# Performance work log

Hardware: AMD Instinct MI355X
Metric: run time of the kernel (lower is better)

The kernel has to match this reference:

```python
import jax, jax.numpy as jnp
import numpy as np

DIM = 768
HEADS = 12
DH = DIM // HEADS
HIDDEN = 4 * DIM
EPS = 1e-5


def layernorm(x, g, b):
    mu = jnp.mean(x, axis=-1, keepdims=True)
    var = jnp.mean(jnp.square(x - mu), axis=-1, keepdims=True)
    return (x - mu) * jax.lax.rsqrt(var + EPS) * g + b


def setup_inputs() -> dict:
    key = jax.random.key(0)
    ks = jax.random.split(key, 12)
    B, N = 8, 1024
    s_in = 1.0 / np.sqrt(DIM)
    s_hid = 1.0 / np.sqrt(HIDDEN)
    return {
        "x": jax.random.normal(ks[0], (B, N, DIM), jnp.float32),
        "q_extra": jax.random.normal(ks[1], (B, N, DIM), jnp.float32),
        "ln1_g": jnp.ones((DIM,), jnp.float32),
        "ln1_b": jnp.zeros((DIM,), jnp.float32),
        "w_kv": jax.random.normal(ks[2], (DIM, 2 * DIM), jnp.float32) * s_in,
        "w_out": jax.random.normal(ks[3], (DIM, DIM), jnp.float32) * s_in,
        "b_out": jnp.zeros((DIM,), jnp.float32),
        "ln2_g": jnp.ones((DIM,), jnp.float32),
        "ln2_b": jnp.zeros((DIM,), jnp.float32),
        "w1": jax.random.normal(ks[4], (DIM, HIDDEN), jnp.float32) * s_in,
        "b1": jnp.zeros((HIDDEN,), jnp.float32),
        "w2": jax.random.normal(ks[5], (HIDDEN, DIM), jnp.float32) * s_hid,
        "b2": jnp.zeros((DIM,), jnp.float32),
    }


def reference(x, q_extra, ln1_g, ln1_b, w_kv, w_out, b_out, ln2_g, ln2_b, w1, b1, w2, b2):
    B, N, C = x.shape
    scale = DH ** (-0.5)

    # pre-norm cross attention
    xn = layernorm(x, ln1_g, ln1_b)
    kv = (xn @ w_kv).reshape(B, N, 2, HEADS, DH)
    k = kv[:, :, 0]  # [B,N,H,Dh]
    v = kv[:, :, 1]
    q = q_extra.reshape(B, N, HEADS, DH)
    dots = jnp.einsum('bnhd,bmhd->bhnm', q, k) * scale
    attn = jax.nn.softmax(dots, axis=-1)
    out = jnp.einsum('bhnm,bmhd->bnhd', attn, v).reshape(B, N, C)
    out = out @ w_out + b_out

    x = x + out  # residual

    # pre-norm MLP
    h = layernorm(x, ln2_g, ln2_b)
    h = jax.nn.gelu(h @ w1 + b1, approximate=False)
    h = h @ w2 + b2
    return x + h
```

## Files before the change

kernel.cpp:

```cpp
#include <hip/hip_runtime.h>
#include <math.h>

typedef __attribute__((ext_vector_type(8))) short short8;
typedef __attribute__((ext_vector_type(8))) _Float16 half8;
typedef __attribute__((ext_vector_type(2))) __fp16 fp16x2;
typedef __attribute__((ext_vector_type(4))) float float4v;
typedef __attribute__((ext_vector_type(4))) unsigned short ushort4v;

__device__ __forceinline__ unsigned short f2bf(float f) {
  union { unsigned int i; float f; } x; x.f = f;
  unsigned int r = x.i + 0x7fffu + ((x.i >> 16) & 1u);
  return (unsigned short)(r >> 16);
}

__device__ __forceinline__ float gelu_f(float y) {
  const float z = fabsf(y) * 0.70710678118654752f;
  const float t = 1.0f / (1.0f + 0.3275911f * z);
  const float poly = t * (0.254829592f + t * (-0.284496736f +
                     t * (1.421413741f + t * (-1.453152027f + t * 1.061405429f))));
  const float e = exp2f(-z * z * 1.44269504088896f);
  const float erfz = copysignf(1.0f - poly * e, y);
  return 0.5f * y * (1.0f + erfz);
}

__global__ void ln_kernel(const float* __restrict__ in, const float* __restrict__ g,
                          const float* __restrict__ b, unsigned short* __restrict__ out) {
  const int wave = threadIdx.x >> 6, lane = threadIdx.x & 63;
  const int row = blockIdx.x * 4 + wave;
  const float* xr = in + (size_t)row * 768 + lane * 4;
  const float4 v0 = *(const float4*)(xr);
  const float4 v1 = *(const float4*)(xr + 256);
  const float4 v2 = *(const float4*)(xr + 512);
  float s  = (v0.x + v0.y) + (v0.z + v0.w) + (v1.x + v1.y) + (v1.z + v1.w)
           + (v2.x + v2.y) + (v2.z + v2.w);
  float s2 = v0.x*v0.x + v0.y*v0.y + v0.z*v0.z + v0.w*v0.w
           + v1.x*v1.x + v1.y*v1.y + v1.z*v1.z + v1.w*v1.w
           + v2.x*v2.x + v2.y*v2.y + v2.z*v2.z + v2.w*v2.w;
  for (int off = 32; off > 0; off >>= 1) {
    s  += __shfl_xor(s, off, 64);
    s2 += __shfl_xor(s2, off, 64);
  }
  const float mu = s * (1.0f / 768.0f);
  const float var = s2 * (1.0f / 768.0f) - mu * mu;
  const float rstd = rsqrtf(var + 1e-5f);
  const float* gp = g + lane * 4;
  const float* bp = b + lane * 4;
  unsigned short* orow = out + (size_t)row * 768 + lane * 4;
#pragma unroll
  for (int k = 0; k < 3; ++k) {
    const float4 v = (k == 0) ? v0 : (k == 1) ? v1 : v2;
    const float4 gv = *(const float4*)(gp + k * 256);
    const float4 bv = *(const float4*)(bp + k * 256);
    ushort4v o;
    o.x = f2bf((v.x - mu) * rstd * gv.x + bv.x);
    o.y = f2bf((v.y - mu) * rstd * gv.y + bv.y);
    o.z = f2bf((v.z - mu) * rstd * gv.z + bv.z);
    o.w = f2bf((v.w - mu) * rstd * gv.w + bv.w);
    *(ushort4v*)(orow + k * 256) = o;
  }
}

__global__ void wtrans_kernel(const float* __restrict__ in, unsigned short* __restrict__ out,
                              int K, int N) {
  __shared__ float tile[32][33];
  const int k0 = blockIdx.y * 32, n0 = blockIdx.x * 32;
  const int tr = threadIdx.x >> 5, tc = threadIdx.x & 31;
#pragma unroll
  for (int i = 0; i < 4; ++i)
    tile[tr + i * 8][tc] = in[(size_t)(k0 + tr + i * 8) * N + n0 + tc];
  __syncthreads();
#pragma unroll
  for (int i = 0; i < 4; ++i)
    out[(size_t)(n0 + tr + i * 8) * K + k0 + tc] = f2bf(tile[tc][tr + i * 8]);
}

#define SWIZ_BLOCK(GX, TW)                                        \
  const int _id = (int)blockIdx.x;                                \
  const int _gy8 = (int)gridDim.x / (8 * (GX));                   \
  const int _xcd = _id & 7, _jj = _id >> 3;                       \
  const int row0 = (_xcd * _gy8 + _jj / (GX)) * 128;              \
  const int col0 = (_jj % (GX)) * (TW);

#define ASM_FENCE asm volatile("" ::: "memory")

__device__ __forceinline__ void gemm128(
    const unsigned short* __restrict__ A, int lda,
    const unsigned short* __restrict__ Bt, int ldb, int K,
    int row0, int col0,
    unsigned short* As, unsigned short* Bs,
    float4v acc[4][4]) {
  const int t = threadIdx.x, lane = t & 63, wave = t >> 6;
  const int quad = lane >> 4, l16 = lane & 15;
  const int wr = wave >> 1, wc = wave & 1;
  const int srow = lane >> 3;
  const int scol = ((lane & 7) ^ srow) * 8;
#pragma unroll
  for (int mt = 0; mt < 4; ++mt)
#pragma unroll
    for (int nt = 0; nt < 4; ++nt) acc[mt][nt] = (float4v)(0.0f);

  for (int kk = 0; kk < K; kk += 64) {
    __syncthreads();
#pragma unroll
    for (int j = 0; j < 4; ++j) {
      const int chunk = wave * 4 + j;
      const int r = chunk * 8 + srow;
      __builtin_amdgcn_global_load_lds(
          (const __attribute__((address_space(1))) unsigned int*)(A + (size_t)(row0 + r) * lda + kk + scol),
          (__attribute__((address_space(3))) unsigned int*)(As + chunk * 512),
          16, 0, 0);
      __builtin_amdgcn_global_load_lds(
          (const __attribute__((address_space(1))) unsigned int*)(Bt + (size_t)(col0 + r) * ldb + kk + scol),
          (__attribute__((address_space(3))) unsigned int*)(Bs + chunk * 512),
          16, 0, 0);
    }
    __syncthreads();
#pragma unroll
    for (int ks = 0; ks < 2; ++ks) {
      const int gsw = ((ks * 4 + quad) ^ (l16 & 7)) * 8;
      short8 af[4], bfv[4];
#pragma unroll
      for (int i = 0; i < 4; ++i) {
        af[i]  = *(const short8*)(As + (wr * 64 + i * 16 + l16) * 64 + gsw);
        bfv[i] = *(const short8*)(Bs + (wc * 64 + i * 16 + l16) * 64 + gsw);
      }
#pragma unroll
      for (int mt = 0; mt < 4; ++mt)
#pragma unroll
        for (int nt = 0; nt < 4; ++nt)
          acc[mt][nt] = __builtin_amdgcn_mfma_f32_16x16x32_bf16(af[mt], bfv[nt], acc[mt][nt], 0, 0, 0);
    }
  }
}

#define GEMM128_PROLOGUE(GX)                                     \
  __shared__ unsigned short As[128 * 64];                        \
  __shared__ unsigned short Bs[128 * 64];                        \
  float4v acc[4][4];                                             \
  SWIZ_BLOCK(GX, 128)                                            \
  const int t = threadIdx.x, lane = t & 63, wave = t >> 6;       \
  const int quad = lane >> 4, l16 = lane & 15;                   \
  const int wr = wave >> 1, wc = wave & 1; (void)t;

__device__ __forceinline__ void stage12864(
    const unsigned short* __restrict__ A, int lda,
    const unsigned short* __restrict__ Bt, int ldb,
    int row0, int col0, int kk,
    unsigned short* Asb, unsigned short* Bsb,
    int wave, int srow, int scol) {
#pragma unroll
  for (int j = 0; j < 4; ++j) {
    const int chunk = wave * 4 + j;
    const int r = chunk * 8 + srow;
    __builtin_amdgcn_global_load_lds(
        (const __attribute__((address_space(1))) unsigned int*)(A + (size_t)(row0 + r) * lda + kk + scol),
        (__attribute__((address_space(3))) unsigned int*)(Asb + chunk * 512),
        16, 0, 0);
  }
#pragma unroll
  for (int j = 0; j < 2; ++j) {
    const int chunk = wave * 2 + j;
    const int r = chunk * 8 + srow;
    __builtin_amdgcn_global_load_lds(
        (const __attribute__((address_space(1))) unsigned int*)(Bt + (size_t)(col0 + r) * ldb + kk + scol),
        (__attribute__((address_space(3))) unsigned int*)(Bsb + chunk * 512),
        16, 0, 0);
  }
}

__device__ __forceinline__ void mfma_step12864(
    const unsigned short* Ab, const unsigned short* Bb,
    int wave, int quad, int l16, float4v acc[2][4]) {
#pragma unroll
  for (int ks = 0; ks < 2; ++ks) {
    const int gsw = ((ks * 4 + quad) ^ (l16 & 7)) * 8;
    short8 af[2], bfv[4];
#pragma unroll
    for (int i = 0; i < 2; ++i)
      af[i] = *(const short8*)(Ab + (wave * 32 + i * 16 + l16) * 64 + gsw);
#pragma unroll
    for (int i = 0; i < 4; ++i)
      bfv[i] = *(const short8*)(Bb + (i * 16 + l16) * 64 + gsw);
#pragma unroll
    for (int mt = 0; mt < 2; ++mt)
#pragma unroll
      for (int nt = 0; nt < 4; ++nt)
        acc[mt][nt] = __builtin_amdgcn_mfma_f32_16x16x32_bf16(af[mt], bfv[nt], acc[mt][nt], 0, 0, 0);
  }
}

__device__ __forceinline__ void gemm12864(
    const unsigned short* __restrict__ A, int lda,
    const unsigned short* __restrict__ Bt, int ldb, int K,
    int row0, int col0,
    unsigned short* As, unsigned short* Bs,
    float4v acc[2][4]) {
  const int t = threadIdx.x, lane = t & 63, wave = t >> 6;
  const int quad = lane >> 4, l16 = lane & 15;
  const int srow = lane >> 3;
  const int scol = ((lane & 7) ^ srow) * 8;
#pragma unroll
  for (int mt = 0; mt < 2; ++mt)
#pragma unroll
    for (int nt = 0; nt < 4; ++nt) acc[mt][nt] = (float4v)(0.0f);

  stage12864(A, lda, Bt, ldb, row0, col0, 0, As, Bs, wave, srow, scol);
  stage12864(A, lda, Bt, ldb, row0, col0, 64, As + 8192, Bs + 4096, wave, srow, scol);

  for (int kk = 0; kk < K - 128; kk += 128) {
    asm volatile("s_waitcnt vmcnt(6)" ::: "memory");
    __builtin_amdgcn_s_barrier();
    ASM_FENCE;
    mfma_step12864(As, Bs, wave, quad, l16, acc);
    ASM_FENCE;
    __builtin_amdgcn_s_barrier();
    ASM_FENCE;
    stage12864(A, lda, Bt, ldb, row0, col0, kk + 128, As, Bs, wave, srow, scol);

    asm volatile("s_waitcnt vmcnt(6)" ::: "memory");
    __builtin_amdgcn_s_barrier();
    ASM_FENCE;
    mfma_step12864(As + 8192, Bs + 4096, wave, quad, l16, acc);
    ASM_FENCE;
    __builtin_amdgcn_s_barrier();
    ASM_FENCE;
    stage12864(A, lda, Bt, ldb, row0, col0, kk + 192, As + 8192, Bs + 4096, wave, srow, scol);
  }
  asm volatile("s_waitcnt vmcnt(6)" ::: "memory");
  __builtin_amdgcn_s_barrier();
  ASM_FENCE;
  mfma_step12864(As, Bs, wave, quad, l16, acc);
  asm volatile("s_waitcnt vmcnt(0)" ::: "memory");
  __builtin_amdgcn_s_barrier();
  ASM_FENCE;
  mfma_step12864(As + 8192, Bs + 4096, wave, quad, l16, acc);
}

#define GEMM12864_PROLOGUE(GX)                                   \
  __shared__ unsigned short As[2 * 128 * 64];                    \
  __shared__ unsigned short Bs[2 * 64 * 64];                     \
  float4v acc[2][4];                                             \
  SWIZ_BLOCK(GX, 64)                                             \
  const int t = threadIdx.x, lane = t & 63, wave = t >> 6;       \
  const int quad = lane >> 4, l16 = lane & 15; (void)t;

__global__ void gemm_kv_kernel(const unsigned short* __restrict__ xn,
                               const unsigned short* __restrict__ wkvt,
                               _Float16* __restrict__ kbuf,
                               _Float16* __restrict__ vtbuf) {
  GEMM128_PROLOGUE(12)
  gemm128(xn, 768, wkvt, 768, 768, row0, col0, As, Bs, acc);
#pragma unroll
  for (int mt = 0; mt < 4; ++mt)
#pragma unroll
    for (int nt = 0; nt < 4; ++nt) {
      const int j = col0 + wc * 64 + nt * 16 + l16;
#pragma unroll
      for (int r = 0; r < 4; ++r) {
        const int m = row0 + wr * 64 + mt * 16 + quad * 4 + r;
        const int bb = m >> 10, n = m & 1023;
        const float c = acc[mt][nt][r];
        if (j < 768) {
          const int hh = j >> 6, d = j & 63;
          kbuf[((size_t)(bb * 12 + hh) * 1024 + n) * 64 + d] = (_Float16)c;
        } else {
          const int j2 = j - 768, hh = j2 >> 6, d = j2 & 63;
          vtbuf[((size_t)(bb * 12 + hh) * 64 + d) * 1024 + n] = (_Float16)c;
        }
      }
    }
}

#define AST 72
#define PST 72
__global__ __launch_bounds__(256, 3)
void attn_kernel(const float* __restrict__ q_extra,
                 const _Float16* __restrict__ kbuf,
                 const _Float16* __restrict__ vtbuf,
                 unsigned short* __restrict__ ao) {
  __shared__ _Float16 Ks[64 * AST];
  __shared__ _Float16 Vs[64 * AST];
  __shared__ _Float16 Ps[4][2][16 * PST];
  const int id = (int)blockIdx.x;
  const int pair = id % 96, qb = id / 96;
  const int h = pair >> 3, b = pair & 7;
  const int q0 = qb * 128;
  const int t = threadIdx.x, lane = t & 63, wave = t >> 6;
  const int quad = lane >> 4, l16 = lane & 15;

  const float QS = 0.125f * 1.44269504088896f;
  half8 qf[2][2];
#pragma unroll
  for (int qs = 0; qs < 2; ++qs) {
    const float* qp = q_extra +
        ((size_t)((b * 1024 + q0 + wave * 32 + qs * 16 + l16) * 12 + h)) * 64 + quad * 8;
    float4 a0 = *(const float4*)(qp);
    float4 a1 = *(const float4*)(qp + 4);
    float4 c0 = *(const float4*)(qp + 32);
    float4 c1 = *(const float4*)(qp + 36);
    union { fp16x2 h2[4]; half8 h8; } u0, u1;
    u0.h2[0] = __builtin_amdgcn_cvt_pkrtz(a0.x * QS, a0.y * QS);
    u0.h2[1] = __builtin_amdgcn_cvt_pkrtz(a0.z * QS, a0.w * QS);
    u0.h2[2] = __builtin_amdgcn_cvt_pkrtz(a1.x * QS, a1.y * QS);
    u0.h2[3] = __builtin_amdgcn_cvt_pkrtz(a1.z * QS, a1.w * QS);
    u1.h2[0] = __builtin_amdgcn_cvt_pkrtz(c0.x * QS, c0.y * QS);
    u1.h2[1] = __builtin_amdgcn_cvt_pkrtz(c0.z * QS, c0.w * QS);
    u1.h2[2] = __builtin_amdgcn_cvt_pkrtz(c1.x * QS, c1.y * QS);
    u1.h2[3] = __builtin_amdgcn_cvt_pkrtz(c1.z * QS, c1.w * QS);
    qf[qs][0] = u0.h8; qf[qs][1] = u1.h8;
  }

  const _Float16* kb = kbuf + (size_t)(b * 12 + h) * 65536;
  const _Float16* vb = vtbuf + (size_t)(b * 12 + h) * 65536;
  const int srow = t >> 2, su = (t & 3) * 16;

  half8 kp0 = *(const half8*)(kb + (size_t)srow * 64 + su);
  half8 kp1 = *(const half8*)(kb + (size_t)srow * 64 + su + 8);
  half8 vp0 = *(const half8*)(vb + (size_t)srow * 1024 + su);
  half8 vp1 = *(const half8*)(vb + (size_t)srow * 1024 + su + 8);

  float m_s[2] = {-1e30f, -1e30f}, l_s[2] = {0.0f, 0.0f};
  float4v acc[2][4];
#pragma unroll
  for (int qs = 0; qs < 2; ++qs)
#pragma unroll
    for (int nt = 0; nt < 4; ++nt) acc[qs][nt] = (float4v)(0.0f);

  for (int c = 0; c < 16; ++c) {
    __syncthreads();
    *(half8*)(Ks + srow * AST + su)     = kp0;
    *(half8*)(Ks + srow * AST + su + 8) = kp1;
    *(half8*)(Vs + srow * AST + su)     = vp0;
    *(half8*)(Vs + srow * AST + su + 8) = vp1;
    if (c < 15) {
      const int key1 = (c + 1) * 64;
      kp0 = *(const half8*)(kb + (size_t)(key1 + srow) * 64 + su);
      kp1 = *(const half8*)(kb + (size_t)(key1 + srow) * 64 + su + 8);
      vp0 = *(const half8*)(vb + (size_t)srow * 1024 + key1 + su);
      vp1 = *(const half8*)(vb + (size_t)srow * 1024 + key1 + su + 8);
    }
    __syncthreads();

#pragma unroll
    for (int qs = 0; qs < 2; ++qs) {
      float4v s[4];
#pragma unroll
      for (int kt = 0; kt < 4; ++kt) {
        const _Float16* kr = Ks + (kt * 16 + l16) * AST;
        half8 kf0 = *(const half8*)(kr + quad * 8);
        half8 kf1 = *(const half8*)(kr + 32 + quad * 8);
        float4v a = (float4v)(0.f);
        a = __builtin_amdgcn_mfma_f32_16x16x32_f16(kf0, qf[qs][0], a, 0, 0, 0);
        a = __builtin_amdgcn_mfma_f32_16x16x32_f16(kf1, qf[qs][1], a, 0, 0, 0);
        s[kt] = a;
      }

      float mx = fmaxf(fmaxf(fmaxf(s[0][0], s[0][1]), fmaxf(s[0][2], s[0][3])),
                       fmaxf(fmaxf(s[1][0], s[1][1]), fmaxf(s[1][2], s[1][3])));
      mx = fmaxf(mx, fmaxf(fmaxf(fmaxf(s[2][0], s[2][1]), fmaxf(s[2][2], s[2][3])),
                           fmaxf(fmaxf(s[3][0], s[3][1]), fmaxf(s[3][2], s[3][3]))));
      mx = fmaxf(mx, __shfl_xor(mx, 16, 64));
      mx = fmaxf(mx, __shfl_xor(mx, 32, 64));

      if (!__all(mx <= m_s[qs] + 8.0f)) {
        const float mn = fmaxf(m_s[qs], mx);
        const float alpha = exp2f(m_s[qs] - mn);
        m_s[qs] = mn;
        l_s[qs] *= alpha;
        float ab[4];
#pragma unroll
        for (int r = 0; r < 4; ++r) ab[r] = __shfl(alpha, quad * 4 + r, 64);
#pragma unroll
        for (int nt = 0; nt < 4; ++nt)
#pragma unroll
          for (int r = 0; r < 4; ++r) acc[qs][nt][r] *= ab[r];
      }

      _Float16* pw = Ps[wave][qs];
      float sum = 0.0f;
#pragma unroll
      for (int kt = 0; kt < 4; ++kt) {
        const float p0 = exp2f(s[kt][0] - m_s[qs]);
        const float p1 = exp2f(s[kt][1] - m_s[qs]);
        const float p2 = exp2f(s[kt][2] - m_s[qs]);
        const float p3 = exp2f(s[kt][3] - m_s[qs]);
        sum += (p0 + p1) + (p2 + p3);
        union { fp16x2 h2[2]; uint2 u; } pk;
        pk.h2[0] = __builtin_amdgcn_cvt_pkrtz(p0, p1);
        pk.h2[1] = __builtin_amdgcn_cvt_pkrtz(p2, p3);
        *(uint2*)(pw + l16 * PST + kt * 16 + quad * 4) = pk.u;
      }
      sum += __shfl_xor(sum, 16, 64);
      sum += __shfl_xor(sum, 32, 64);
      l_s[qs] += sum;

      half8 pf0 = *(const half8*)(pw + l16 * PST + quad * 8);
      half8 pf1 = *(const half8*)(pw + l16 * PST + 32 + quad * 8);
#pragma unroll
      for (int nt = 0; nt < 4; ++nt) {
        const _Float16* vr = Vs + (nt * 16 + l16) * AST;
        half8 vf0 = *(const half8*)(vr + quad * 8);
        half8 vf1 = *(const half8*)(vr + 32 + quad * 8);
        acc[qs][nt] = __builtin_amdgcn_mfma_f32_16x16x32_f16(pf0, vf0, acc[qs][nt], 0, 0, 0);
        acc[qs][nt] = __builtin_amdgcn_mfma_f32_16x16x32_f16(pf1, vf1, acc[qs][nt], 0, 0, 0);
      }
    }
  }

#pragma unroll
  for (int qs = 0; qs < 2; ++qs) {
    const float inv = 1.0f / l_s[qs];
    float ib[4];
#pragma unroll
    for (int r = 0; r < 4; ++r) ib[r] = __shfl(inv, quad * 4 + r, 64);
#pragma unroll
    for (int nt = 0; nt < 4; ++nt) {
#pragma unroll
      for (int r = 0; r < 4; ++r) {
        const int m = q0 + wave * 32 + qs * 16 + quad * 4 + r;
        ao[(size_t)(b * 1024 + m) * 768 + h * 64 + nt * 16 + l16] =
            f2bf(acc[qs][nt][r] * ib[r]);
      }
    }
  }
}

__global__ void gemm_outproj_kernel(const unsigned short* __restrict__ ao,
                                    const unsigned short* __restrict__ woutt,
                                    const float* __restrict__ b_out,
                                    const float* __restrict__ x,
                                    float* __restrict__ x2) {
  GEMM12864_PROLOGUE(12)
  gemm12864(ao, 768, woutt, 768, 768, row0, col0, As, Bs, acc);
#pragma unroll
  for (int mt = 0; mt < 2; ++mt)
#pragma unroll
    for (int nt = 0; nt < 4; ++nt) {
      const int j = col0 + nt * 16 + l16;
#pragma unroll
      for (int r = 0; r < 4; ++r) {
        const int m = row0 + wave * 32 + mt * 16 + quad * 4 + r;
        const size_t idx = (size_t)m * 768 + j;
        x2[idx] = acc[mt][nt][r] + b_out[j] + x[idx];
      }
    }
}

__global__ void gemm_mlp1_kernel(const unsigned short* __restrict__ h,
                                 const unsigned short* __restrict__ w1t,
                                 const float* __restrict__ b1,
                                 unsigned short* __restrict__ h1) {
  GEMM128_PROLOGUE(24)
  gemm128(h, 768, w1t, 768, 768, row0, col0, As, Bs, acc);
#pragma unroll
  for (int mt = 0; mt < 4; ++mt)
#pragma unroll
    for (int nt = 0; nt < 4; ++nt) {
      const int j = col0 + wc * 64 + nt * 16 + l16;
#pragma unroll
      for (int r = 0; r < 4; ++r) {
        const int m = row0 + wr * 64 + mt * 16 + quad * 4 + r;
        const float y = acc[mt][nt][r] + b1[j];
        h1[(size_t)m * 3072 + j] = f2bf(gelu_f(y));
      }
    }
}

__global__ void gemm_mlp2_kernel(const unsigned short* __restrict__ h1,
                                 const unsigned short* __restrict__ w2t,
                                 const float* __restrict__ b2,
                                 const float* __restrict__ x2,
                                 float* __restrict__ out) {
  GEMM12864_PROLOGUE(12)
  gemm12864(h1, 3072, w2t, 3072, 3072, row0, col0, As, Bs, acc);
#pragma unroll
  for (int mt = 0; mt < 2; ++mt)
#pragma unroll
    for (int nt = 0; nt < 4; ++nt) {
      const int j = col0 + nt * 16 + l16;
#pragma unroll
      for (int r = 0; r < 4; ++r) {
        const int m = row0 + wave * 32 + mt * 16 + quad * 4 + r;
        const size_t idx = (size_t)m * 768 + j;
        out[idx] = acc[mt][nt][r] + b2[j] + x2[idx];
      }
    }
}

extern "C" void kernel_launch(void* const* d_in, const int* in_sizes, int n_in,
                              void* d_out, int out_size, void* d_ws, size_t ws_size,
                              hipStream_t stream) {
  const float* x       = (const float*)d_in[0];
  const float* q_extra = (const float*)d_in[1];
  const float* ln1_g   = (const float*)d_in[2];
  const float* ln1_b   = (const float*)d_in[3];
  const float* w_kv    = (const float*)d_in[4];
  const float* w_out   = (const float*)d_in[5];
  const float* b_out   = (const float*)d_in[6];
  const float* ln2_g   = (const float*)d_in[7];
  const float* ln2_b   = (const float*)d_in[8];
  const float* w1      = (const float*)d_in[9];
  const float* b1      = (const float*)d_in[10];
  const float* w2      = (const float*)d_in[11];
  const float* b2      = (const float*)d_in[12];
  float* out = (float*)d_out;

  char* ws = (char*)d_ws;
  unsigned short* xn    = (unsigned short*)(ws);
  _Float16*       kbuf  = (_Float16*)(ws + 12582912);
  _Float16*       vtbuf = (_Float16*)(ws + 25165824);
  unsigned short* ao    = (unsigned short*)(ws + 37748736);
  float*          x2    = (float*)(ws + 50331648);
  unsigned short* h1    = (unsigned short*)(ws + 75497472);
  unsigned short* hbuf  = xn;
  unsigned short* wkvt  = ao;
  unsigned short* woutt = h1;
  unsigned short* w1t   = (unsigned short*)kbuf;
  unsigned short* w2t   = (unsigned short*)vtbuf;

  ln_kernel<<<2048, 256, 0, stream>>>(x, ln1_g, ln1_b, xn);
  wtrans_kernel<<<dim3(48, 24), 256, 0, stream>>>(w_kv, wkvt, 768, 1536);
  wtrans_kernel<<<dim3(24, 24), 256, 0, stream>>>(w_out, woutt, 768, 768);
  gemm_kv_kernel<<<768, 256, 0, stream>>>(xn, wkvt, kbuf, vtbuf);
  attn_kernel<<<768, 256, 0, stream>>>(q_extra, kbuf, vtbuf, ao);
  wtrans_kernel<<<dim3(96, 24), 256, 0, stream>>>(w1, w1t, 768, 3072);
  wtrans_kernel<<<dim3(24, 96), 256, 0, stream>>>(w2, w2t, 3072, 768);
  gemm_outproj_kernel<<<768, 256, 0, stream>>>(ao, woutt, b_out, x, x2);
  ln_kernel<<<2048, 256, 0, stream>>>(x2, ln2_g, ln2_b, hbuf);
  gemm_mlp1_kernel<<<1536, 256, 0, stream>>>(hbuf, w1t, b1, h1);
  gemm_mlp2_kernel<<<768, 256, 0, stream>>>(h1, w2t, b2, x2, out);
}
```

Baseline: 354.4 us.

## Retile MLP1 GEMM to 256x128 with direct-to-LDS loads; tune attention softmax

The MLP1 GEMM is rewritten as a 512-thread, 256x128-tile kernel. It uses global_load_lds direct-to-LDS copies with an XOR-swizzled layout and XCD-aware block mapping, which halves the grid and doubles reuse of each B tile. In the attention kernel, the per-step row-max and row-sum cross-lane shuffles are deferred or made conditional: the sum reduction moves to the epilogue, and the max reduction runs only when rescaling. MFMA sections are wrapped in s_setprio to favour matrix issue. The new GEMM relies on launch bounds and a single-buffered loop without prefetch, which may limit latency hiding.

```diff
diff --git a/kernel.cpp b/kernel.cpp
--- a/kernel.cpp
+++ b/kernel.cpp
@@ -344,6 +344,7 @@
 #pragma unroll
     for (int qs = 0; qs < 2; ++qs) {
       float4v s[4];
+      __builtin_amdgcn_s_setprio(1);
 #pragma unroll
       for (int kt = 0; kt < 4; ++kt) {
         const _Float16* kr = Ks + (kt * 16 + l16) * AST;
@@ -354,16 +355,20 @@
         a = __builtin_amdgcn_mfma_f32_16x16x32_f16(kf1, qf[qs][1], a, 0, 0, 0);
         s[kt] = a;
       }
-
-      float mx = fmaxf(fmaxf(fmaxf(s[0][0], s[0][1]), fmaxf(s[0][2], s[0][3])),
-                       fmaxf(fmaxf(s[1][0], s[1][1]), fmaxf(s[1][2], s[1][3])));
-      mx = fmaxf(mx, fmaxf(fmaxf(fmaxf(s[2][0], s[2][1]), fmaxf(s[2][2], s[2][3])),
-                           fmaxf(fmaxf(s[3][0], s[3][1]), fmaxf(s[3][2], s[3][3]))));
-      mx = fmaxf(mx, __shfl_xor(mx, 16, 64));
-      mx = fmaxf(mx, __shfl_xor(mx, 32, 64));
-
-      if (!__all(mx <= m_s[qs] + 8.0f)) {
-        const float mn = fmaxf(m_s[qs], mx);
+      __builtin_amdgcn_s_setprio(0);
+
+      const float t1 = fmaxf(fmaxf(s[0][0], s[0][1]), s[0][2]);
+      const float t2 = fmaxf(fmaxf(s[0][3], s[1][0]), s[1][1]);
+      const float t3 = fmaxf(fmaxf(s[1][2], s[1][3]), s[2][0]);
+      const float t4 = fmaxf(fmaxf(s[2][1], s[2][2]), s[2][3]);
+      const float t5 = fmaxf(fmaxf(s[3][0], s[3][1]), s[3][2]);
+      const float mx = fmaxf(fmaxf(fmaxf(t1, t2), t3),
+                             fmaxf(fmaxf(t4, t5), s[3][3]));
+
+      if (__any(mx > m_s[qs] + 8.0f)) {
+        float gm = fmaxf(mx, __shfl_xor(mx, 16, 64));
+        gm = fmaxf(gm, __shfl_xor(gm, 32, 64));
+        const float mn = fmaxf(m_s[qs], gm);
         const float alpha = exp2f(m_s[qs] - mn);
         m_s[qs] = mn;
         l_s[qs] *= alpha;
@@ -390,12 +395,11 @@
         pk.h2[1] = __builtin_amdgcn_cvt_pkrtz(p2, p3);
         *(uint2*)(pw + l16 * PST + kt * 16 + quad * 4) = pk.u;
       }
-      sum += __shfl_xor(sum, 16, 64);
-      sum += __shfl_xor(sum, 32, 64);
       l_s[qs] += sum;
 
       half8 pf0 = *(const half8*)(pw + l16 * PST + quad * 8);
       half8 pf1 = *(const half8*)(pw + l16 * PST + 32 + quad * 8);
+      __builtin_amdgcn_s_setprio(1);
 #pragma unroll
       for (int nt = 0; nt < 4; ++nt) {
         const _Float16* vr = Vs + (nt * 16 + l16) * AST;
@@ -404,11 +408,14 @@
         acc[qs][nt] = __builtin_amdgcn_mfma_f32_16x16x32_f16(pf0, vf0, acc[qs][nt], 0, 0, 0);
         acc[qs][nt] = __builtin_amdgcn_mfma_f32_16x16x32_f16(pf1, vf1, acc[qs][nt], 0, 0, 0);
       }
+      __builtin_amdgcn_s_setprio(0);
     }
   }
 
 #pragma unroll
   for (int qs = 0; qs < 2; ++qs) {
+    l_s[qs] += __shfl_xor(l_s[qs], 16, 64);
+    l_s[qs] += __shfl_xor(l_s[qs], 32, 64);
     const float inv = 1.0f / l_s[qs];
     float ib[4];
 #pragma unroll
@@ -446,12 +453,66 @@
     }
 }
 
-__global__ void gemm_mlp1_kernel(const unsigned short* __restrict__ h,
-                                 const unsigned short* __restrict__ w1t,
-                                 const float* __restrict__ b1,
-                                 unsigned short* __restrict__ h1) {
-  GEMM128_PROLOGUE(24)
-  gemm128(h, 768, w1t, 768, 768, row0, col0, As, Bs, acc);
+__global__ __launch_bounds__(512, 6)
+void gemm_mlp1_kernel(const unsigned short* __restrict__ h,
+                      const unsigned short* __restrict__ w1t,
+                      const float* __restrict__ b1,
+                      unsigned short* __restrict__ h1) {
+  __shared__ unsigned short As[256 * 64];
+  __shared__ unsigned short Bs[128 * 64];
+  float4v acc[4][4];
+  const int _id = (int)blockIdx.x;
+  const int _xcd = _id & 7, _jj = _id >> 3;
+  const int row0 = (_xcd * 4 + _jj / 24) * 256;
+  const int col0 = (_jj % 24) * 128;
+  const int t = threadIdx.x, lane = t & 63, wave = t >> 6;
+  const int quad = lane >> 4, l16 = lane & 15;
+  const int wr = wave >> 1, wc = wave & 1;
+  const int srow = lane >> 3;
+  const int scol = ((lane & 7) ^ srow) * 8;
+#pragma unroll
+  for (int mt = 0; mt < 4; ++mt)
+#pragma unroll
+    for (int nt = 0; nt < 4; ++nt) acc[mt][nt] = (float4v)(0.0f);
+
+  for (int kk = 0; kk < 768; kk += 64) {
+    __syncthreads();
+#pragma unroll
+    for (int j = 0; j < 4; ++j) {
+      const int chunk = wave * 4 + j;
+      const int r = chunk * 8 + srow;
+      __builtin_amdgcn_global_load_lds(
+          (const __attribute__((address_space(1))) unsigned int*)(h + (size_t)(row0 + r) * 768 + kk + scol),
+          (__attribute__((address_space(3))) unsigned int*)(As + chunk * 512),
+          16, 0, 0);
+    }
+#pragma unroll
+    for (int j = 0; j < 2; ++j) {
+      const int chunk = wave * 2 + j;
+      const int r = chunk * 8 + srow;
+      __builtin_amdgcn_global_load_lds(
+          (const __attribute__((address_space(1))) unsigned int*)(w1t + (size_t)(col0 + r) * 768 + kk + scol),
+          (__attribute__((address_space(3))) unsigned int*)(Bs + chunk * 512),
+          16, 0, 0);
+    }
+    __syncthreads();
+#pragma unroll
+    for (int ks = 0; ks < 2; ++ks) {
+      const int gsw = ((ks * 4 + quad) ^ (l16 & 7)) * 8;
+      short8 af[4], bfv[4];
+#pragma unroll
+      for (int i = 0; i < 4; ++i) {
+        af[i]  = *(const short8*)(As + (wr * 64 + i * 16 + l16) * 64 + gsw);
+        bfv[i] = *(const short8*)(Bs + (wc * 64 + i * 16 + l16) * 64 + gsw);
+      }
+#pragma unroll
+      for (int mt = 0; mt < 4; ++mt)
+#pragma unroll
+        for (int nt = 0; nt < 4; ++nt)
+          acc[mt][nt] = __builtin_amdgcn_mfma_f32_16x16x32_bf16(af[mt], bfv[nt], acc[mt][nt], 0, 0, 0);
+    }
+  }
+
 #pragma unroll
   for (int mt = 0; mt < 4; ++mt)
 #pragma unroll
@@ -527,6 +588,6 @@
   wtrans_kernel<<<dim3(24, 96), 256, 0, stream>>>(w2, w2t, 3072, 768);
   gemm_outproj_kernel<<<768, 256, 0, stream>>>(ao, woutt, b_out, x, x2);
   ln_kernel<<<2048, 256, 0, stream>>>(x2, ln2_g, ln2_b, hbuf);
-  gemm_mlp1_kernel<<<1536, 256, 0, stream>>>(hbuf, w1t, b1, h1);
+  gemm_mlp1_kernel<<<768, 512, 0, stream>>>(hbuf, w1t, b1, h1);
   gemm_mlp2_kernel<<<768, 256, 0, stream>>>(h1, w2t, b2, x2, out);
 }
```

Result: slower. 647.7 us (+82.8%).

## Double-buffer 128x128 GEMM with K=32 stages and tune attention softmax scheduling

Applied to the files above, without the earlier changes.

The 128x128 GEMM used by the KV and MLP1 kernels is replaced by a double-buffered variant that stages K in 32-wide slices with a new XOR swizzle. It waits on partial vmcnt so global-to-LDS loads overlap MFMA work instead of serialising behind two full barriers per 64-wide step. In attention, the row-max cross-lane shuffles now run only when some lane needs a rescale, and the row-sum shuffle reduction moves out of the key loop to the end. s_setprio is raised around the MFMA blocks. The changes add barrier-ordering complexity and depend on per-lane partial sums staying consistent with a shared rescale decision.

```diff
diff --git a/kernel.cpp b/kernel.cpp
--- a/kernel.cpp
+++ b/kernel.cpp
@@ -83,7 +83,49 @@
 
 #define ASM_FENCE asm volatile("" ::: "memory")
 
-__device__ __forceinline__ void gemm128(
+__device__ __forceinline__ void stage12832(
+    const unsigned short* __restrict__ A, int lda,
+    const unsigned short* __restrict__ Bt, int ldb,
+    int row0, int col0, int kk,
+    unsigned short* Asb, unsigned short* Bsb,
+    int wave, int srow4, int gcol) {
+#pragma unroll
+  for (int j = 0; j < 2; ++j) {
+    const int chunk = wave * 2 + j;
+    const int r = chunk * 16 + srow4;
+    __builtin_amdgcn_global_load_lds(
+        (const __attribute__((address_space(1))) unsigned int*)(A + (size_t)(row0 + r) * lda + kk + gcol),
+        (__attribute__((address_space(3))) unsigned int*)(Asb + chunk * 512),
+        16, 0, 0);
+  }
+#pragma unroll
+  for (int j = 0; j < 2; ++j) {
+    const int chunk = wave * 2 + j;
+    const int r = chunk * 16 + srow4;
+    __builtin_amdgcn_global_load_lds(
+        (const __attribute__((address_space(1))) unsigned int*)(Bt + (size_t)(col0 + r) * ldb + kk + gcol),
+        (__attribute__((address_space(3))) unsigned int*)(Bsb + chunk * 512),
+        16, 0, 0);
+  }
+}
+
+__device__ __forceinline__ void mfma_step12832(
+    const unsigned short* Ab, const unsigned short* Bb,
+    int wr, int wc, int rblk, int l16, float4v acc[4][4]) {
+  short8 af[4], bfv[4];
+#pragma unroll
+  for (int i = 0; i < 4; ++i) {
+    af[i]  = *(const short8*)(Ab + (wr * 64 + i * 16 + l16) * 32 + rblk);
+    bfv[i] = *(const short8*)(Bb + (wc * 64 + i * 16 + l16) * 32 + rblk);
+  }
+#pragma unroll
+  for (int mt = 0; mt < 4; ++mt)
+#pragma unroll
+    for (int nt = 0; nt < 4; ++nt)
+      acc[mt][nt] = __builtin_amdgcn_mfma_f32_16x16x32_bf16(af[mt], bfv[nt], acc[mt][nt], 0, 0, 0);
+}
+
+__device__ __forceinline__ void gemm12832(
     const unsigned short* __restrict__ A, int lda,
     const unsigned short* __restrict__ Bt, int ldb, int K,
     int row0, int col0,
@@ -92,50 +134,49 @@
   const int t = threadIdx.x, lane = t & 63, wave = t >> 6;
   const int quad = lane >> 4, l16 = lane & 15;
   const int wr = wave >> 1, wc = wave & 1;
-  const int srow = lane >> 3;
-  const int scol = ((lane & 7) ^ srow) * 8;
+  const int srow4 = lane >> 2;
+  const int gcol = (((lane & 3) ^ ((srow4 >> 1) & 3))) * 8;
+  const int rblk = (quad ^ ((l16 >> 1) & 3)) * 8;
 #pragma unroll
   for (int mt = 0; mt < 4; ++mt)
 #pragma unroll
     for (int nt = 0; nt < 4; ++nt) acc[mt][nt] = (float4v)(0.0f);
 
-  for (int kk = 0; kk < K; kk += 64) {
-    __syncthreads();
-#pragma unroll
-    for (int j = 0; j < 4; ++j) {
-      const int chunk = wave * 4 + j;
-      const int r = chunk * 8 + srow;
-      __builtin_amdgcn_global_load_lds(
-          (const __attribute__((address_space(1))) unsigned int*)(A + (size_t)(row0 + r) * lda + kk + scol),
-          (__attribute__((address_space(3))) unsigned int*)(As + chunk * 512),
-          16, 0, 0);
-      __builtin_amdgcn_global_load_lds(
-          (const __attribute__((address_space(1))) unsigned int*)(Bt + (size_t)(col0 + r) * ldb + kk + scol),
-          (__attribute__((address_space(3))) unsigned int*)(Bs + chunk * 512),
-          16, 0, 0);
-    }
-    __syncthreads();
-#pragma unroll
-    for (int ks = 0; ks < 2; ++ks) {
-      const int gsw = ((ks * 4 + quad) ^ (l16 & 7)) * 8;
-      short8 af[4], bfv[4];
-#pragma unroll
-      for (int i = 0; i < 4; ++i) {
-        af[i]  = *(const short8*)(As + (wr * 64 + i * 16 + l16) * 64 + gsw);
-        bfv[i] = *(const short8*)(Bs + (wc * 64 + i * 16 + l16) * 64 + gsw);
-      }
-#pragma unroll
-      for (int mt = 0; mt < 4; ++mt)
-#pragma unroll
-        for (int nt = 0; nt < 4; ++nt)
-          acc[mt][nt] = __builtin_amdgcn_mfma_f32_16x16x32_bf16(af[mt], bfv[nt], acc[mt][nt], 0, 0, 0);
-    }
-  }
-}
-
-#define GEMM128_PROLOGUE(GX)                                     \
-  __shared__ unsigned short As[128 * 64];                        \
-  __shared__ unsigned short Bs[128 * 64];                        \
+  stage12832(A, lda, Bt, ldb, row0, col0, 0,  As,        Bs,        wave, srow4, gcol);
+  stage12832(A, lda, Bt, ldb, row0, col0, 32, As + 4096, Bs + 4096, wave, srow4, gcol);
+
+  for (int kk = 0; kk < K - 64; kk += 64) {
+    asm volatile("s_waitcnt vmcnt(4)" ::: "memory");
+    __builtin_amdgcn_s_barrier();
+    ASM_FENCE;
+    mfma_step12832(As, Bs, wr, wc, rblk, l16, acc);
+    ASM_FENCE;
+    __builtin_amdgcn_s_barrier();
+    ASM_FENCE;
+    stage12832(A, lda, Bt, ldb, row0, col0, kk + 64, As, Bs, wave, srow4, gcol);
+
+    asm volatile("s_waitcnt vmcnt(4)" ::: "memory");
+    __builtin_amdgcn_s_barrier();
+    ASM_FENCE;
+    mfma_step12832(As + 4096, Bs + 4096, wr, wc, rblk, l16, acc);
+    ASM_FENCE;
+    __builtin_amdgcn_s_barrier();
+    ASM_FENCE;
+    stage12832(A, lda, Bt, ldb, row0, col0, kk + 96, As + 4096, Bs + 4096, wave, srow4, gcol);
+  }
+  asm volatile("s_waitcnt vmcnt(4)" ::: "memory");
+  __builtin_amdgcn_s_barrier();
+  ASM_FENCE;
+  mfma_step12832(As, Bs, wr, wc, rblk, l16, acc);
+  asm volatile("s_waitcnt vmcnt(0)" ::: "memory");
+  __builtin_amdgcn_s_barrier();
+  ASM_FENCE;
+  mfma_step12832(As + 4096, Bs + 4096, wr, wc, rblk, l16, acc);
+}
+
+#define GEMM12832_PROLOGUE(GX)                                   \
+  __shared__ unsigned short As[2 * 128 * 32];                    \
+  __shared__ unsigned short Bs[2 * 128 * 32];                    \
   float4v acc[4][4];                                             \
   SWIZ_BLOCK(GX, 128)                                            \
   const int t = threadIdx.x, lane = t & 63, wave = t >> 6;       \
@@ -248,8 +289,8 @@
                                const unsigned short* __restrict__ wkvt,
                                _Float16* __restrict__ kbuf,
                                _Float16* __restrict__ vtbuf) {
-  GEMM128_PROLOGUE(12)
-  gemm128(xn, 768, wkvt, 768, 768, row0, col0, As, Bs, acc);
+  GEMM12832_PROLOGUE(12)
+  gemm12832(xn, 768, wkvt, 768, 768, row0, col0, As, Bs, acc);
 #pragma unroll
   for (int mt = 0; mt < 4; ++mt)
 #pragma unroll
@@ -344,6 +385,7 @@
 #pragma unroll
     for (int qs = 0; qs < 2; ++qs) {
       float4v s[4];
+      __builtin_amdgcn_s_setprio(1);
 #pragma unroll
       for (int kt = 0; kt < 4; ++kt) {
         const _Float16* kr = Ks + (kt * 16 + l16) * AST;
@@ -354,16 +396,20 @@
         a = __builtin_amdgcn_mfma_f32_16x16x32_f16(kf1, qf[qs][1], a, 0, 0, 0);
         s[kt] = a;
       }
-
-      float mx = fmaxf(fmaxf(fmaxf(s[0][0], s[0][1]), fmaxf(s[0][2], s[0][3])),
-                       fmaxf(fmaxf(s[1][0], s[1][1]), fmaxf(s[1][2], s[1][3])));
-      mx = fmaxf(mx, fmaxf(fmaxf(fmaxf(s[2][0], s[2][1]), fmaxf(s[2][2], s[2][3])),
-                           fmaxf(fmaxf(s[3][0], s[3][1]), fmaxf(s[3][2], s[3][3]))));
-      mx = fmaxf(mx, __shfl_xor(mx, 16, 64));
-      mx = fmaxf(mx, __shfl_xor(mx, 32, 64));
-
-      if (!__all(mx <= m_s[qs] + 8.0f)) {
-        const float mn = fmaxf(m_s[qs], mx);
+      __builtin_amdgcn_s_setprio(0);
+
+      const float t1 = fmaxf(fmaxf(s[0][0], s[0][1]), s[0][2]);
+      const float t2 = fmaxf(fmaxf(s[0][3], s[1][0]), s[1][1]);
+      const float t3 = fmaxf(fmaxf(s[1][2], s[1][3]), s[2][0]);
+      const float t4 = fmaxf(fmaxf(s[2][1], s[2][2]), s[2][3]);
+      const float t5 = fmaxf(fmaxf(s[3][0], s[3][1]), s[3][2]);
+      const float mx = fmaxf(fmaxf(fmaxf(t1, t2), t3),
+                             fmaxf(fmaxf(t4, t5), s[3][3]));
+
+      if (__any(mx > m_s[qs] + 8.0f)) {
+        float gm = fmaxf(mx, __shfl_xor(mx, 16, 64));
+        gm = fmaxf(gm, __shfl_xor(gm, 32, 64));
+        const float mn = fmaxf(m_s[qs], gm);
         const float alpha = exp2f(m_s[qs] - mn);
         m_s[qs] = mn;
         l_s[qs] *= alpha;
@@ -390,12 +436,11 @@
         pk.h2[1] = __builtin_amdgcn_cvt_pkrtz(p2, p3);
         *(uint2*)(pw + l16 * PST + kt * 16 + quad * 4) = pk.u;
       }
-      sum += __shfl_xor(sum, 16, 64);
-      sum += __shfl_xor(sum, 32, 64);
       l_s[qs] += sum;
 
       half8 pf0 = *(const half8*)(pw + l16 * PST + quad * 8);
       half8 pf1 = *(const half8*)(pw + l16 * PST + 32 + quad * 8);
+      __builtin_amdgcn_s_setprio(1);
 #pragma unroll
       for (int nt = 0; nt < 4; ++nt) {
         const _Float16* vr = Vs + (nt * 16 + l16) * AST;
@@ -404,11 +449,14 @@
         acc[qs][nt] = __builtin_amdgcn_mfma_f32_16x16x32_f16(pf0, vf0, acc[qs][nt], 0, 0, 0);
         acc[qs][nt] = __builtin_amdgcn_mfma_f32_16x16x32_f16(pf1, vf1, acc[qs][nt], 0, 0, 0);
       }
+      __builtin_amdgcn_s_setprio(0);
     }
   }
 
 #pragma unroll
   for (int qs = 0; qs < 2; ++qs) {
+    l_s[qs] += __shfl_xor(l_s[qs], 16, 64);
+    l_s[qs] += __shfl_xor(l_s[qs], 32, 64);
     const float inv = 1.0f / l_s[qs];
     float ib[4];
 #pragma unroll
@@ -450,8 +498,8 @@
                                  const unsigned short* __restrict__ w1t,
                                  const float* __restrict__ b1,
                                  unsigned short* __restrict__ h1) {
-  GEMM128_PROLOGUE(24)
-  gemm128(h, 768, w1t, 768, 768, row0, col0, As, Bs, acc);
+  GEMM12832_PROLOGUE(24)
+  gemm12832(h, 768, w1t, 768, 768, row0, col0, As, Bs, acc);
 #pragma unroll
   for (int mt = 0; mt < 4; ++mt)
 #pragma unroll
```

Result: slower. 375.4 us (+5.9%).

## Merge weight-transpose launches and restructure attention softmax with deferred row-sum reduction

Applied to the files above, without the earlier changes.

Pairs of weight-transpose launches are merged into one kernel that dispatches blocks to either matrix by block index, which removes two launches. In the attention loop, the QK MFMAs for both query slices are issued together under raised wave priority. The max cross-lane shuffle now runs only inside the rescale branch, and the row-sum shuffles are moved out of the loop to the final normalization, since per-lane partial sums can be combined once at the end. The cost is more live registers for the score arrays, plus any interaction of the setprio hints with scheduling.

```diff
diff --git a/kernel.cpp b/kernel.cpp
--- a/kernel.cpp
+++ b/kernel.cpp
@@ -60,10 +60,17 @@
   }
 }
 
-__global__ void wtrans_kernel(const float* __restrict__ in, unsigned short* __restrict__ out,
-                              int K, int N) {
+__global__ void wtrans2_kernel(const float* __restrict__ inA, unsigned short* __restrict__ outA,
+                               int KA, int NA, int bxA, int nA,
+                               const float* __restrict__ inB, unsigned short* __restrict__ outB,
+                               int KB, int NB, int bxB) {
+  int id = (int)blockIdx.x;
+  const float* in; unsigned short* out; int K, N, bx, by;
+  if (id < nA) { in = inA; out = outA; K = KA; N = NA; bx = id % bxA; by = id / bxA; }
+  else { id -= nA; in = inB; out = outB; K = KB; N = NB; bx = id % bxB; by = id / bxB; }
+  (void)K;
   __shared__ float tile[32][33];
-  const int k0 = blockIdx.y * 32, n0 = blockIdx.x * 32;
+  const int k0 = by * 32, n0 = bx * 32;
   const int tr = threadIdx.x >> 5, tc = threadIdx.x & 31;
 #pragma unroll
   for (int i = 0; i < 4; ++i)
@@ -341,9 +348,10 @@
     }
     __syncthreads();
 
-#pragma unroll
-    for (int qs = 0; qs < 2; ++qs) {
-      float4v s[4];
+    float4v s[2][4];
+    __builtin_amdgcn_s_setprio(1);
+#pragma unroll
+    for (int qs = 0; qs < 2; ++qs)
 #pragma unroll
       for (int kt = 0; kt < 4; ++kt) {
         const _Float16* kr = Ks + (kt * 16 + l16) * AST;
@@ -352,18 +360,24 @@
         float4v a = (float4v)(0.f);
         a = __builtin_amdgcn_mfma_f32_16x16x32_f16(kf0, qf[qs][0], a, 0, 0, 0);
         a = __builtin_amdgcn_mfma_f32_16x16x32_f16(kf1, qf[qs][1], a, 0, 0, 0);
-        s[kt] = a;
-      }
-
-      float mx = fmaxf(fmaxf(fmaxf(s[0][0], s[0][1]), fmaxf(s[0][2], s[0][3])),
-                       fmaxf(fmaxf(s[1][0], s[1][1]), fmaxf(s[1][2], s[1][3])));
-      mx = fmaxf(mx, fmaxf(fmaxf(fmaxf(s[2][0], s[2][1]), fmaxf(s[2][2], s[2][3])),
-                           fmaxf(fmaxf(s[3][0], s[3][1]), fmaxf(s[3][2], s[3][3]))));
-      mx = fmaxf(mx, __shfl_xor(mx, 16, 64));
-      mx = fmaxf(mx, __shfl_xor(mx, 32, 64));
-
-      if (!__all(mx <= m_s[qs] + 8.0f)) {
-        const float mn = fmaxf(m_s[qs], mx);
+        s[qs][kt] = a;
+      }
+    __builtin_amdgcn_s_setprio(0);
+
+#pragma unroll
+    for (int qs = 0; qs < 2; ++qs) {
+      const float t1 = fmaxf(fmaxf(s[qs][0][0], s[qs][0][1]), s[qs][0][2]);
+      const float t2 = fmaxf(fmaxf(s[qs][0][3], s[qs][1][0]), s[qs][1][1]);
+      const float t3 = fmaxf(fmaxf(s[qs][1][2], s[qs][1][3]), s[qs][2][0]);
+      const float t4 = fmaxf(fmaxf(s[qs][2][1], s[qs][2][2]), s[qs][2][3]);
+      const float t5 = fmaxf(fmaxf(s[qs][3][0], s[qs][3][1]), s[qs][3][2]);
+      const float mx = fmaxf(fmaxf(fmaxf(t1, t2), t3),
+                             fmaxf(fmaxf(t4, t5), s[qs][3][3]));
+
+      if (__any(mx > m_s[qs] + 8.0f)) {
+        float gm = fmaxf(mx, __shfl_xor(mx, 16, 64));
+        gm = fmaxf(gm, __shfl_xor(gm, 32, 64));
+        const float mn = fmaxf(m_s[qs], gm);
         const float alpha = exp2f(m_s[qs] - mn);
         m_s[qs] = mn;
         l_s[qs] *= alpha;
@@ -380,22 +394,25 @@
       float sum = 0.0f;
 #pragma unroll
       for (int kt = 0; kt < 4; ++kt) {
-        const float p0 = exp2f(s[kt][0] - m_s[qs]);
-        const float p1 = exp2f(s[kt][1] - m_s[qs]);
-        const float p2 = exp2f(s[kt][2] - m_s[qs]);
-        const float p3 = exp2f(s[kt][3] - m_s[qs]);
+        const float p0 = exp2f(s[qs][kt][0] - m_s[qs]);
+        const float p1 = exp2f(s[qs][kt][1] - m_s[qs]);
+        const float p2 = exp2f(s[qs][kt][2] - m_s[qs]);
+        const float p3 = exp2f(s[qs][kt][3] - m_s[qs]);
         sum += (p0 + p1) + (p2 + p3);
         union { fp16x2 h2[2]; uint2 u; } pk;
         pk.h2[0] = __builtin_amdgcn_cvt_pkrtz(p0, p1);
         pk.h2[1] = __builtin_amdgcn_cvt_pkrtz(p2, p3);
         *(uint2*)(pw + l16 * PST + kt * 16 + quad * 4) = pk.u;
       }
-      sum += __shfl_xor(sum, 16, 64);
-      sum += __shfl_xor(sum, 32, 64);
       l_s[qs] += sum;
-
+    }
+
+#pragma unroll
+    for (int qs = 0; qs < 2; ++qs) {
+      _Float16* pw = Ps[wave][qs];
       half8 pf0 = *(const half8*)(pw + l16 * PST + quad * 8);
       half8 pf1 = *(const half8*)(pw + l16 * PST + 32 + quad * 8);
+      __builtin_amdgcn_s_setprio(1);
 #pragma unroll
       for (int nt = 0; nt < 4; ++nt) {
         const _Float16* vr = Vs + (nt * 16 + l16) * AST;
@@ -404,11 +421,14 @@
         acc[qs][nt] = __builtin_amdgcn_mfma_f32_16x16x32_f16(pf0, vf0, acc[qs][nt], 0, 0, 0);
         acc[qs][nt] = __builtin_amdgcn_mfma_f32_16x16x32_f16(pf1, vf1, acc[qs][nt], 0, 0, 0);
       }
+      __builtin_amdgcn_s_setprio(0);
     }
   }
 
 #pragma unroll
   for (int qs = 0; qs < 2; ++qs) {
+    l_s[qs] += __shfl_xor(l_s[qs], 16, 64);
+    l_s[qs] += __shfl_xor(l_s[qs], 32, 64);
     const float inv = 1.0f / l_s[qs];
     float ib[4];
 #pragma unroll
@@ -519,12 +539,12 @@
   unsigned short* w2t   = (unsigned short*)vtbuf;
 
   ln_kernel<<<2048, 256, 0, stream>>>(x, ln1_g, ln1_b, xn);
-  wtrans_kernel<<<dim3(48, 24), 256, 0, stream>>>(w_kv, wkvt, 768, 1536);
-  wtrans_kernel<<<dim3(24, 24), 256, 0, stream>>>(w_out, woutt, 768, 768);
+  wtrans2_kernel<<<1728, 256, 0, stream>>>(w_kv, wkvt, 768, 1536, 48, 1152,
+                                           w_out, woutt, 768, 768, 24);
   gemm_kv_kernel<<<768, 256, 0, stream>>>(xn, wkvt, kbuf, vtbuf);
   attn_kernel<<<768, 256, 0, stream>>>(q_extra, kbuf, vtbuf, ao);
-  wtrans_kernel<<<dim3(96, 24), 256, 0, stream>>>(w1, w1t, 768, 3072);
-  wtrans_kernel<<<dim3(24, 96), 256, 0, stream>>>(w2, w2t, 3072, 768);
+  wtrans2_kernel<<<4608, 256, 0, stream>>>(w1, w1t, 768, 3072, 96, 2304,
+                                           w2, w2t, 3072, 768, 24);
   gemm_outproj_kernel<<<768, 256, 0, stream>>>(ao, woutt, b_out, x, x2);
   ln_kernel<<<2048, 256, 0, stream>>>(x2, ln2_g, ln2_b, hbuf);
   gemm_mlp1_kernel<<<1536, 256, 0, stream>>>(hbuf, w1t, b1, h1);
```

Measured after the change: 360.2 us. About the same (+1.6%).
